# Kernel optimization log

Measured on AMD Instinct MI355X. Metric: run time of the kernel, lower is better.

The kernel has to match this reference:

```python
import math
import jax, jax.numpy as jnp
import numpy as np

B, DIM, L = 2, 512, 2048
H = 16
HD = DIM // H  # 32
R = 32
K = 3
GAMMA = 1.0


def _conv1d(x, w, b=None):
    # x: [B, Cin, L], w: [Cout, Cin, K] -> [B, Cout, L_out] (VALID)
    out = jax.lax.conv_general_dilated(
        x, w, window_strides=(1,), padding='VALID',
        dimension_numbers=('NCH', 'OIH', 'NCH'))
    if b is not None:
        out = out + b[None, :, None]
    return out


def _sketch_p4(x, G1, G2):
    # x: [B, H, L, HD]; G1, G2: [HD, R]
    # p=4: half = (1/sqrt(r)) * (x@G1 * x@G2); return half*half
    half = (x @ G1) * (x @ G2) / math.sqrt(R)
    return half * half  # [B, H, L, R]


def setup_inputs() -> dict:
    key = jax.random.key(0)
    ks = jax.random.split(key, 12)
    x = jax.random.normal(ks[0], (B, DIM, L), dtype=jnp.float32)
    # conv / linear params (kaiming-ish scale)
    q_w = jax.random.normal(ks[1], (DIM, DIM, K), dtype=jnp.float32) / math.sqrt(DIM * K)
    q_b = jnp.zeros((DIM,), dtype=jnp.float32)
    k_w = jax.random.normal(ks[2], (DIM, DIM, K), dtype=jnp.float32) / math.sqrt(DIM * K)
    k_b = jnp.zeros((DIM,), dtype=jnp.float32)
    v_w = jax.random.normal(ks[3], (DIM, DIM, 1), dtype=jnp.float32) / math.sqrt(DIM)
    proj_w = jax.random.normal(ks[4], (DIM, DIM), dtype=jnp.float32) / math.sqrt(DIM)
    proj_b = jnp.zeros((DIM,), dtype=jnp.float32)
    # learnable scalars
    gamma_q = jnp.ones((1,), dtype=jnp.float32) * GAMMA
    beta_q = jnp.zeros((1,), dtype=jnp.float32)
    gamma_k = jnp.ones((1,), dtype=jnp.float32) * GAMMA
    beta_k = jnp.zeros((1,), dtype=jnp.float32)
    # sketch matrices, std = 1/sqrt(r)
    G1q = jax.random.normal(ks[5], (HD, R), dtype=jnp.float32) / math.sqrt(R)
    G2q = jax.random.normal(ks[6], (HD, R), dtype=jnp.float32) / math.sqrt(R)
    G1k = jax.random.normal(ks[7], (HD, R), dtype=jnp.float32) / math.sqrt(R)
    G2k = jax.random.normal(ks[8], (HD, R), dtype=jnp.float32) / math.sqrt(R)
    return dict(x=x, q_w=q_w, q_b=q_b, k_w=k_w, k_b=k_b, v_w=v_w,
                proj_w=proj_w, proj_b=proj_b,
                gamma_q=gamma_q, beta_q=beta_q, gamma_k=gamma_k, beta_k=beta_k,
                G1q=G1q, G2q=G2q, G1k=G1k, G2k=G2k)


def reference(x, q_w, q_b, k_w, k_b, v_w, proj_w, proj_b,
              gamma_q, beta_q, gamma_k, beta_k, G1q, G2q, G1k, G2k):
    batch, dim, length = x.shape
    # causal left pad by K-1
    x_pad = jnp.pad(x, ((0, 0), (0, 0), (K - 1, 0)))
    q = _conv1d(x_pad, q_w, q_b)   # [B, DIM, L]
    k = _conv1d(x_pad, k_w, k_b)   # [B, DIM, L]
    v = _conv1d(x, v_w)            # [B, DIM, L] (1x1 conv, no bias)

    def shape(t):
        # [B, DIM, L] -> [B, H, HD, L] -> [B, H, L, HD]
        return t.reshape(batch, H, HD, length).transpose(0, 1, 3, 2)

    q, k, v = shape(q), shape(k), shape(v)
    q = gamma_q * q + beta_q
    k = gamma_k * k + beta_k
    phi_q = _sketch_p4(q, G1q, G2q)  # [B, H, L, R]
    phi_k = _sketch_p4(k, G1k, G2k)  # [B, H, L, R]
    scores = jnp.einsum('bhlr,bhmr->bhlm', phi_q, phi_k)  # [B, H, L, L]
    attn = scores / (scores.sum(axis=-1, keepdims=True) + 1e-6)
    o = jnp.einsum('bhlm,bhmd->bhld', attn, v)  # [B, H, L, HD]
    # [B, H, L, HD] -> [B, H, HD, L] -> [B, DIM, L] -> [B, L, DIM]
    o = o.transpose(0, 1, 3, 2).reshape(batch, dim, length).transpose(0, 2, 1)
    return o @ proj_w.T + proj_b
```

## Files before the change

### kernel.cpp

```cpp
#include <hip/hip_runtime.h>
#include <hip/hip_bf16.h>

#define DIMC 512
#define LEN  2048
#define NH   16
#define HD   32
#define RR   32

typedef __bf16 bf8_t __attribute__((ext_vector_type(8)));
typedef float  f4_t  __attribute__((ext_vector_type(4)));

__device__ __forceinline__ void gload16(const void* g, void* l) {
    __builtin_amdgcn_global_load_lds(
        (const __attribute__((address_space(1))) unsigned int*)g,
        (__attribute__((address_space(3))) unsigned int*)l, 16, 0, 0);
}

__global__ __launch_bounds__(256) void split_x_kernel(
    const float* __restrict__ x, __bf16* __restrict__ xTh, __bf16* __restrict__ xTl)
{
    __shared__ float tile[64][65];
    const int b  = blockIdx.z;
    const int l0 = blockIdx.x * 64;
    const int c0 = blockIdx.y * 64;
    const int tid = threadIdx.x;
    #pragma unroll
    for (int it = 0; it < 4; ++it) {
        int cl = (tid >> 4) + it * 16;
        int ll = (tid & 15) * 4;
        float4 v4 = *reinterpret_cast<const float4*>(
            x + ((size_t)b * DIMC + c0 + cl) * LEN + l0 + ll);
        tile[cl][ll+0] = v4.x; tile[cl][ll+1] = v4.y;
        tile[cl][ll+2] = v4.z; tile[cl][ll+3] = v4.w;
    }
    __syncthreads();
    const int lr = tid >> 2;
    const int cb = (tid & 3) * 16;
    size_t base = ((size_t)b * 2050 + l0 + lr + 2) * DIMC + c0 + cb;
    #pragma unroll
    for (int e = 0; e < 16; ++e) {
        float f = tile[cb + e][lr];
        __bf16 h = (__bf16)f;
        xTh[base + e] = h;
        xTl[base + e] = (__bf16)(f - (float)h);
    }
    if (blockIdx.x == 0 && blockIdx.y == 0) {
        size_t pb = (size_t)b * 2050 * DIMC;
        #pragma unroll
        for (int e = 0; e < 4; ++e) {
            int p = tid * 4 + e;
            xTh[pb + p] = (__bf16)0.f;
            xTl[pb + p] = (__bf16)0.f;
        }
    }
}

__global__ __launch_bounds__(256) void split_w_kernel(
    const float* __restrict__ qw, const float* __restrict__ kw,
    const float* __restrict__ vw, __bf16* __restrict__ Wrh, __bf16* __restrict__ Wrl)
{
    int idx = blockIdx.x * 256 + threadIdx.x;
    int m   = idx / 1536;
    int rem = idx - m * 1536;
    int kk  = rem >> 9;
    int ci  = rem & 511;
    float f;
    if (m < 512)       f = qw[((size_t)m * 512 + ci) * 3 + kk];
    else if (m < 1024) f = kw[((size_t)(m - 512) * 512 + ci) * 3 + kk];
    else               f = (kk == 2) ? vw[(size_t)(m - 1024) * 512 + ci] : 0.f;
    __bf16 h = (__bf16)f;
    Wrh[idx] = h;
    Wrl[idx] = (__bf16)(f - (float)h);
}

__global__ __launch_bounds__(256) void split_pw_kernel(
    const float* __restrict__ pw, __bf16* __restrict__ pwh, __bf16* __restrict__ pwl)
{
    int idx = blockIdx.x * 256 + threadIdx.x;
    float f = pw[idx];
    __bf16 h = (__bf16)f;
    pwh[idx] = h;
    pwl[idx] = (__bf16)(f - (float)h);
}

__global__ __launch_bounds__(256) void conv_mfma_kernel(
    const __bf16* __restrict__ xTh, const __bf16* __restrict__ xTl,
    const __bf16* __restrict__ Wrh, const __bf16* __restrict__ Wrl,
    const float* __restrict__ q_b, const float* __restrict__ k_b,
    float* __restrict__ q, float* __restrict__ k, float* __restrict__ v,
    int m_off, int kks)
{
    __shared__ __bf16 sAh[128 * 32], sAl[128 * 32], sBh[64 * 32], sBl[64 * 32];
    const int b   = blockIdx.z;
    const int mg  = m_off + blockIdx.y * 128;
    const int n0  = blockIdx.x * 64;
    const int tid = threadIdx.x;
    const int wave = tid >> 6, lane = tid & 63;
    const int wm = wave >> 1, wn = wave & 1;
    const int lr = lane & 15, k8 = lane >> 4;

    const __bf16* xh = xTh + (size_t)b * 2050 * DIMC;
    const __bf16* xl = xTl + (size_t)b * 2050 * DIMC;

    f4_t acc[4][2];
    #pragma unroll
    for (int i = 0; i < 4; ++i)
        #pragma unroll
        for (int j = 0; j < 2; ++j)
            #pragma unroll
            for (int e = 0; e < 4; ++e) acc[i][j][e] = 0.f;

    const int sr0 = tid >> 2;
    const int ss  = tid & 3;
    const int sk0 = ((ss ^ ((sr0 >> 1) & 3)) << 3);
    const int sr1 = sr0 + 64;
    const int sk1 = ((ss ^ ((sr1 >> 1) & 3)) << 3);

    for (int kk = kks; kk < 3; ++kk) {
        const __bf16* wAh = Wrh + (size_t)mg * 1536 + kk * 512;
        const __bf16* wAl = Wrl + (size_t)mg * 1536 + kk * 512;
        const __bf16* xbh = xh + (size_t)(n0 + kk) * DIMC;
        const __bf16* xbl = xl + (size_t)(n0 + kk) * DIMC;
        for (int k0 = 0; k0 < 512; k0 += 32) {
            gload16(wAh + (size_t)sr0 * 1536 + k0 + sk0, (char*)sAh + tid * 16);
            gload16(wAh + (size_t)sr1 * 1536 + k0 + sk1, (char*)sAh + (256 + tid) * 16);
            gload16(wAl + (size_t)sr0 * 1536 + k0 + sk0, (char*)sAl + tid * 16);
            gload16(wAl + (size_t)sr1 * 1536 + k0 + sk1, (char*)sAl + (256 + tid) * 16);
            gload16(xbh + (size_t)sr0 * DIMC + k0 + sk0, (char*)sBh + tid * 16);
            gload16(xbl + (size_t)sr0 * DIMC + k0 + sk0, (char*)sBl + tid * 16);
            __syncthreads();
            bf8_t ah[4], al[4], bh[2], bl[2];
            #pragma unroll
            for (int i = 0; i < 4; ++i) {
                int row = wm * 64 + i * 16 + lr;
                int off = row * 64 + ((k8 ^ ((row >> 1) & 3)) << 4);
                ah[i] = *(const bf8_t*)((const char*)sAh + off);
                al[i] = *(const bf8_t*)((const char*)sAl + off);
            }
            #pragma unroll
            for (int j = 0; j < 2; ++j) {
                int row = wn * 32 + j * 16 + lr;
                int off = row * 64 + ((k8 ^ ((row >> 1) & 3)) << 4);
                bh[j] = *(const bf8_t*)((const char*)sBh + off);
                bl[j] = *(const bf8_t*)((const char*)sBl + off);
            }
            #pragma unroll
            for (int i = 0; i < 4; ++i)
                #pragma unroll
                for (int j = 0; j < 2; ++j) {
                    acc[i][j] = __builtin_amdgcn_mfma_f32_16x16x32_bf16(ah[i], bh[j], acc[i][j], 0, 0, 0);
                    acc[i][j] = __builtin_amdgcn_mfma_f32_16x16x32_bf16(ah[i], bl[j], acc[i][j], 0, 0, 0);
                    acc[i][j] = __builtin_amdgcn_mfma_f32_16x16x32_bf16(al[i], bh[j], acc[i][j], 0, 0, 0);
                }
            __syncthreads();
        }
    }
    const int sec = mg >> 9;
    float* outp = (sec == 0) ? q : (sec == 1) ? k : v;
    const float* bp = (sec == 0) ? q_b : (sec == 1) ? k_b : nullptr;
    const int cob = mg & 511;
    #pragma unroll
    for (int i = 0; i < 4; ++i)
        #pragma unroll
        for (int r = 0; r < 4; ++r) {
            int co = cob + wm * 64 + i * 16 + k8 * 4 + r;
            float bv = bp ? bp[co] : 0.f;
            float* orow = outp + ((size_t)b * DIMC + co) * LEN;
            #pragma unroll
            for (int j = 0; j < 2; ++j)
                orow[n0 + wn * 32 + j * 16 + lr] = acc[i][j][r] + bv;
        }
}

__global__ __launch_bounds__(256) void proj_mfma_kernel(
    const __bf16* __restrict__ oh, const __bf16* __restrict__ ol,
    const __bf16* __restrict__ pwh, const __bf16* __restrict__ pwl,
    const float* __restrict__ pb, float* __restrict__ out)
{
    __shared__ __bf16 sAh[128 * 32], sAl[128 * 32], sBh[64 * 32], sBl[64 * 32];
    const int m0  = blockIdx.y * 128;
    const int n0  = blockIdx.x * 64;
    const int tid = threadIdx.x;
    const int wave = tid >> 6, lane = tid & 63;
    const int wm = wave >> 1, wn = wave & 1;
    const int lr = lane & 15, k8 = lane >> 4;

    f4_t acc[4][2];
    #pragma unroll
    for (int i = 0; i < 4; ++i)
        #pragma unroll
        for (int j = 0; j < 2; ++j)
            #pragma unroll
            for (int e = 0; e < 4; ++e) acc[i][j][e] = 0.f;

    const int sr0 = tid >> 2;
    const int ss  = tid & 3;
    const int sk0 = ((ss ^ ((sr0 >> 1) & 3)) << 3);
    const int sr1 = sr0 + 64;
    const int sk1 = ((ss ^ ((sr1 >> 1) & 3)) << 3);

    for (int k0 = 0; k0 < 512; k0 += 32) {
        gload16(oh + (size_t)(m0 + sr0) * DIMC + k0 + sk0, (char*)sAh + tid * 16);
        gload16(oh + (size_t)(m0 + sr1) * DIMC + k0 + sk1, (char*)sAh + (256 + tid) * 16);
        gload16(ol + (size_t)(m0 + sr0) * DIMC + k0 + sk0, (char*)sAl + tid * 16);
        gload16(ol + (size_t)(m0 + sr1) * DIMC + k0 + sk1, (char*)sAl + (256 + tid) * 16);
        gload16(pwh + (size_t)(n0 + sr0) * DIMC + k0 + sk0, (char*)sBh + tid * 16);
        gload16(pwl + (size_t)(n0 + sr0) * DIMC + k0 + sk0, (char*)sBl + tid * 16);
        __syncthreads();
        bf8_t ah[4], al[4], bh[2], bl[2];
        #pragma unroll
        for (int i = 0; i < 4; ++i) {
            int row = wm * 64 + i * 16 + lr;
            int off = row * 64 + ((k8 ^ ((row >> 1) & 3)) << 4);
            ah[i] = *(const bf8_t*)((const char*)sAh + off);
            al[i] = *(const bf8_t*)((const char*)sAl + off);
        }
        #pragma unroll
        for (int j = 0; j < 2; ++j) {
            int row = wn * 32 + j * 16 + lr;
            int off = row * 64 + ((k8 ^ ((row >> 1) & 3)) << 4);
            bh[j] = *(const bf8_t*)((const char*)sBh + off);
            bl[j] = *(const bf8_t*)((const char*)sBl + off);
        }
        #pragma unroll
        for (int i = 0; i < 4; ++i)
            #pragma unroll
            for (int j = 0; j < 2; ++j) {
                acc[i][j] = __builtin_amdgcn_mfma_f32_16x16x32_bf16(ah[i], bh[j], acc[i][j], 0, 0, 0);
                acc[i][j] = __builtin_amdgcn_mfma_f32_16x16x32_bf16(ah[i], bl[j], acc[i][j], 0, 0, 0);
                acc[i][j] = __builtin_amdgcn_mfma_f32_16x16x32_bf16(al[i], bh[j], acc[i][j], 0, 0, 0);
            }
        __syncthreads();
    }
    #pragma unroll
    for (int j = 0; j < 2; ++j) {
        int n = n0 + wn * 32 + j * 16 + lr;
        float bv = pb[n];
        #pragma unroll
        for (int i = 0; i < 4; ++i)
            #pragma unroll
            for (int r = 0; r < 4; ++r) {
                int m = m0 + wm * 64 + i * 16 + k8 * 4 + r;
                out[(size_t)m * DIMC + n] = acc[i][j][r] + bv;
            }
    }
}

__global__ __launch_bounds__(256) void sketch_kernel(
    const float* __restrict__ qk, const float* __restrict__ G1,
    const float* __restrict__ G2, const float* __restrict__ gamma,
    const float* __restrict__ beta, float* __restrict__ phi)
{
    __shared__ float g1s[HD][RR];
    __shared__ float g2s[HD][RR];
    __shared__ float qs[8][HD + 1];
    const int b = blockIdx.z, h = blockIdx.y;
    const int l0 = blockIdx.x * 8;
    const int tid = threadIdx.x;
    for (int i = tid; i < HD * RR; i += 256) {
        g1s[i >> 5][i & 31] = G1[i];
        g2s[i >> 5][i & 31] = G2[i];
    }
    const float ga = gamma[0], be = beta[0];
    {
        const int dd = tid >> 3, li = tid & 7;
        qs[li][dd] = ga * qk[((size_t)b * DIMC + h * HD + dd) * LEN + l0 + li] + be;
    }
    __syncthreads();
    const int r = tid & 31, li = tid >> 5;
    float a = 0.f, c = 0.f;
    #pragma unroll
    for (int dd = 0; dd < HD; ++dd) {
        float qv = qs[li][dd];
        a += qv * g1s[dd][r];
        c += qv * g2s[dd][r];
    }
    float hh = a * c * 0.17677669529663687f;
    phi[((size_t)(b * NH + h) * LEN + l0 + li) * RR + r] = hh * hh;
}

__global__ __launch_bounds__(256) void skv_kernel(
    const float* __restrict__ phi_k, const float* __restrict__ v,
    float* __restrict__ Skv, float* __restrict__ sk)
{
    const int b = blockIdx.z, h = blockIdx.y;
    const int l0 = blockIdx.x * 256;
    const int tid = threadIdx.x;
    __shared__ float ps[64][RR];
    __shared__ float vs[64][HD + 1];
    const int r  = tid >> 3;
    const int d4 = (tid & 7) * 4;
    float acc[4] = {0.f, 0.f, 0.f, 0.f};
    float skacc = 0.f;
    const float* pk = phi_k + ((size_t)(b * NH + h) * LEN + l0) * RR;
    const float* vb = v + ((size_t)b * DIMC + h * HD) * LEN + l0;
    for (int c = 0; c < 4; ++c) {
        for (int i = tid; i < 64 * 32; i += 256) {
            ps[i >> 5][i & 31] = pk[c * 64 * 32 + i];
            int dd = i >> 6, lc = i & 63;
            vs[lc][dd] = vb[(size_t)dd * LEN + c * 64 + lc];
        }
        __syncthreads();
        #pragma unroll 8
        for (int lc = 0; lc < 64; ++lc) {
            float pv = ps[lc][r];
            skacc += pv;
            #pragma unroll
            for (int j = 0; j < 4; ++j) acc[j] += pv * vs[lc][d4 + j];
        }
        __syncthreads();
    }
    const size_t base = (size_t)(b * NH + h) * RR + r;
    float* Sp = Skv + base * HD + d4;
    #pragma unroll
    for (int j = 0; j < 4; ++j) atomicAdd(Sp + j, acc[j]);
    if ((tid & 7) == 0) atomicAdd(sk + base, skacc);
}

__global__ __launch_bounds__(256) void onorm_kernel(
    const float* __restrict__ phi_q, const float* __restrict__ Skv,
    const float* __restrict__ sk, __bf16* __restrict__ o_h, __bf16* __restrict__ o_l)
{
    __shared__ float Ss[RR][HD];
    __shared__ float sks[RR];
    __shared__ float ph[8][RR + 1];
    const int b = blockIdx.z, hh = blockIdx.y;
    const int l0 = blockIdx.x * 8;
    const int tid = threadIdx.x;
    const int bh = b * NH + hh;
    for (int i = tid; i < RR * HD; i += 256) Ss[i >> 5][i & 31] = Skv[(size_t)bh * RR * HD + i];
    if (tid < RR) sks[tid] = sk[(size_t)bh * RR + tid];
    {
        const int r = tid & 31, li = tid >> 5;
        ph[li][r] = phi_q[((size_t)bh * LEN + l0 + li) * RR + r];
    }
    __syncthreads();
    const int d = tid & 31, li = tid >> 5;
    float num = 0.f, den = 0.f;
    #pragma unroll
    for (int r = 0; r < RR; ++r) {
        float p = ph[li][r];
        num += p * Ss[r][d];
        den += p * sks[r];
    }
    float val = num / (den + 1e-6f);
    __bf16 hv = (__bf16)val;
    size_t oi = ((size_t)b * LEN + l0 + li) * DIMC + hh * HD + d;
    o_h[oi] = hv;
    o_l[oi] = (__bf16)(val - (float)hv);
}

extern "C" void kernel_launch(void* const* d_in, const int* in_sizes, int n_in,
                              void* d_out, int out_size, void* d_ws, size_t ws_size,
                              hipStream_t stream)
{
    const float* x       = (const float*)d_in[0];
    const float* q_w     = (const float*)d_in[1];
    const float* q_b     = (const float*)d_in[2];
    const float* k_w     = (const float*)d_in[3];
    const float* k_b     = (const float*)d_in[4];
    const float* v_w     = (const float*)d_in[5];
    const float* proj_w  = (const float*)d_in[6];
    const float* proj_b  = (const float*)d_in[7];
    const float* gamma_q = (const float*)d_in[8];
    const float* beta_q  = (const float*)d_in[9];
    const float* gamma_k = (const float*)d_in[10];
    const float* beta_k  = (const float*)d_in[11];
    const float* G1q     = (const float*)d_in[12];
    const float* G2q     = (const float*)d_in[13];
    const float* G1k     = (const float*)d_in[14];
    const float* G2k     = (const float*)d_in[15];

    char* W = (char*)d_ws;
    constexpr size_t QKV   = (size_t)2 * DIMC * LEN * 4;
    constexpr size_t XT    = (size_t)2 * 2050 * DIMC * 2;
    constexpr size_t WR    = (size_t)1536 * 1536 * 2;
    constexpr size_t PW    = (size_t)DIMC * DIMC * 2;
    constexpr size_t SKVB  = (size_t)2 * NH * RR * HD * 4;
    constexpr size_t SKB   = (size_t)2 * NH * RR * 4;

    float*  q    = (float*)(W);
    float*  k    = (float*)(W + QKV);
    float*  v    = (float*)(W + 2 * QKV);
    __bf16* xTh  = (__bf16*)(W + 3 * QKV);
    __bf16* xTl  = (__bf16*)(W + 3 * QKV + XT);
    __bf16* Wrh  = (__bf16*)(W + 3 * QKV + 2 * XT);
    __bf16* Wrl  = (__bf16*)(W + 3 * QKV + 2 * XT + WR);
    __bf16* pwh  = (__bf16*)(W + 3 * QKV + 2 * XT + 2 * WR);
    __bf16* pwl  = (__bf16*)(W + 3 * QKV + 2 * XT + 2 * WR + PW);
    float*  Skv  = (float*)(W + 3 * QKV + 2 * XT + 2 * WR + 2 * PW);
    float*  sk   = (float*)(W + 3 * QKV + 2 * XT + 2 * WR + 2 * PW + SKVB);
    float*  phi_q = (float*)(W + 3 * QKV);
    float*  phi_k = (float*)(W + 3 * QKV + 2 * XT);
    __bf16* o_h   = (__bf16*)(W);
    __bf16* o_l   = (__bf16*)(W + QKV / 2);

    split_x_kernel<<<dim3(LEN / 64, DIMC / 64, 2), 256, 0, stream>>>(x, xTh, xTl);
    split_w_kernel<<<(1536 * 1536) / 256, 256, 0, stream>>>(q_w, k_w, v_w, Wrh, Wrl);
    split_pw_kernel<<<(DIMC * DIMC) / 256, 256, 0, stream>>>(proj_w, pwh, pwl);

    conv_mfma_kernel<<<dim3(LEN / 64, 8, 2), 256, 0, stream>>>(
        xTh, xTl, Wrh, Wrl, q_b, k_b, q, k, v, 0, 0);
    conv_mfma_kernel<<<dim3(LEN / 64, 4, 2), 256, 0, stream>>>(
        xTh, xTl, Wrh, Wrl, q_b, k_b, q, k, v, 1024, 2);

    dim3 sgrid(LEN / 8, NH, 2);
    sketch_kernel<<<sgrid, 256, 0, stream>>>(q, G1q, G2q, gamma_q, beta_q, phi_q);
    sketch_kernel<<<sgrid, 256, 0, stream>>>(k, G1k, G2k, gamma_k, beta_k, phi_k);

    hipMemsetAsync(Skv, 0, SKVB + SKB, stream);
    skv_kernel<<<dim3(LEN / 256, NH, 2), 256, 0, stream>>>(phi_k, v, Skv, sk);

    onorm_kernel<<<sgrid, 256, 0, stream>>>(phi_q, Skv, sk, o_h, o_l);

    proj_mfma_kernel<<<dim3(DIMC / 64, (2 * LEN) / 128), 256, 0, stream>>>(
        o_h, o_l, pwh, pwl, proj_b, (float*)d_out);
}
```

Baseline: 254.9 us.

## Fuse prep kernels and memset into one launch; fuse sketch into conv epilogue

```diff
diff --git a/kernel.cpp b/kernel.cpp
--- a/kernel.cpp
+++ b/kernel.cpp
@@ -16,88 +16,108 @@
         (__attribute__((address_space(3))) unsigned int*)l, 16, 0, 0);
 }
 
-__global__ __launch_bounds__(256) void split_x_kernel(
-    const float* __restrict__ x, __bf16* __restrict__ xTh, __bf16* __restrict__ xTl)
-{
-    __shared__ float tile[64][65];
-    const int b  = blockIdx.z;
-    const int l0 = blockIdx.x * 64;
-    const int c0 = blockIdx.y * 64;
+__global__ __launch_bounds__(256) void prep_kernel(
+    const float* __restrict__ x,
+    const float* __restrict__ qw, const float* __restrict__ kw,
+    const float* __restrict__ vw, const float* __restrict__ pw,
+    __bf16* __restrict__ xTh, __bf16* __restrict__ xTl,
+    __bf16* __restrict__ Wrh, __bf16* __restrict__ Wrl,
+    __bf16* __restrict__ pwh, __bf16* __restrict__ pwl,
+    float* __restrict__ Skv)
+{
+    const int bid = blockIdx.x;
     const int tid = threadIdx.x;
-    #pragma unroll
-    for (int it = 0; it < 4; ++it) {
-        int cl = (tid >> 4) + it * 16;
-        int ll = (tid & 15) * 4;
-        float4 v4 = *reinterpret_cast<const float4*>(
-            x + ((size_t)b * DIMC + c0 + cl) * LEN + l0 + ll);
-        tile[cl][ll+0] = v4.x; tile[cl][ll+1] = v4.y;
-        tile[cl][ll+2] = v4.z; tile[cl][ll+3] = v4.w;
-    }
-    __syncthreads();
-    const int lr = tid >> 2;
-    const int cb = (tid & 3) * 16;
-    size_t base = ((size_t)b * 2050 + l0 + lr + 2) * DIMC + c0 + cb;
-    #pragma unroll
-    for (int e = 0; e < 16; ++e) {
-        float f = tile[cb + e][lr];
+    if (bid < 512) {
+        __shared__ float tile[64][65];
+        const int lblk = bid & 31, cblk = (bid >> 5) & 7, b = bid >> 8;
+        const int l0 = lblk * 64, c0 = cblk * 64;
+        #pragma unroll
+        for (int it = 0; it < 4; ++it) {
+            int cl = (tid >> 4) + it * 16;
+            int ll = (tid & 15) * 4;
+            float4 v4 = *reinterpret_cast<const float4*>(
+                x + ((size_t)b * DIMC + c0 + cl) * LEN + l0 + ll);
+            tile[cl][ll+0] = v4.x; tile[cl][ll+1] = v4.y;
+            tile[cl][ll+2] = v4.z; tile[cl][ll+3] = v4.w;
+        }
+        __syncthreads();
+        const int l  = tid & 63;
+        const int cs = (tid >> 6) * 16;
+        size_t rowbase = ((size_t)b * 2050 + l0 + l + 2) * DIMC + c0;
+        #pragma unroll
+        for (int half = 0; half < 2; ++half) {
+            int c = cs + half * 8;
+            bf8_t hi, lo;
+            #pragma unroll
+            for (int e = 0; e < 8; ++e) {
+                float f = tile[c + e][l];
+                __bf16 h = (__bf16)f;
+                hi[e] = h;
+                lo[e] = (__bf16)(f - (float)h);
+            }
+            *reinterpret_cast<bf8_t*>(xTh + rowbase + c) = hi;
+            *reinterpret_cast<bf8_t*>(xTl + rowbase + c) = lo;
+        }
+        if (lblk == 0 && cblk == 0) {
+            size_t pb = (size_t)b * 2050 * DIMC;
+            #pragma unroll
+            for (int e = 0; e < 4; ++e) {
+                int p = tid * 4 + e;
+                xTh[pb + p] = (__bf16)0.f;
+                xTl[pb + p] = (__bf16)0.f;
+            }
+        }
+    } else if (bid < 9728) {
+        int idx = (bid - 512) * 256 + tid;
+        int m   = idx / 1536;
+        int rem = idx - m * 1536;
+        int kk  = rem >> 9;
+        int ci  = rem & 511;
+        float f;
+        if (m < 512)       f = qw[((size_t)m * 512 + ci) * 3 + kk];
+        else if (m < 1024) f = kw[((size_t)(m - 512) * 512 + ci) * 3 + kk];
+        else               f = (kk == 2) ? vw[(size_t)(m - 1024) * 512 + ci] : 0.f;
         __bf16 h = (__bf16)f;
-        xTh[base + e] = h;
-        xTl[base + e] = (__bf16)(f - (float)h);
-    }
-    if (blockIdx.x == 0 && blockIdx.y == 0) {
-        size_t pb = (size_t)b * 2050 * DIMC;
-        #pragma unroll
-        for (int e = 0; e < 4; ++e) {
-            int p = tid * 4 + e;
-            xTh[pb + p] = (__bf16)0.f;
-            xTl[pb + p] = (__bf16)0.f;
-        }
-    }
-}
-
-__global__ __launch_bounds__(256) void split_w_kernel(
-    const float* __restrict__ qw, const float* __restrict__ kw,
-    const float* __restrict__ vw, __bf16* __restrict__ Wrh, __bf16* __restrict__ Wrl)
-{
-    int idx = blockIdx.x * 256 + threadIdx.x;
-    int m   = idx / 1536;
-    int rem = idx - m * 1536;
-    int kk  = rem >> 9;
-    int ci  = rem & 511;
-    float f;
-    if (m < 512)       f = qw[((size_t)m * 512 + ci) * 3 + kk];
-    else if (m < 1024) f = kw[((size_t)(m - 512) * 512 + ci) * 3 + kk];
-    else               f = (kk == 2) ? vw[(size_t)(m - 1024) * 512 + ci] : 0.f;
-    __bf16 h = (__bf16)f;
-    Wrh[idx] = h;
-    Wrl[idx] = (__bf16)(f - (float)h);
-}
-
-__global__ __launch_bounds__(256) void split_pw_kernel(
-    const float* __restrict__ pw, __bf16* __restrict__ pwh, __bf16* __restrict__ pwl)
-{
-    int idx = blockIdx.x * 256 + threadIdx.x;
-    float f = pw[idx];
-    __bf16 h = (__bf16)f;
-    pwh[idx] = h;
-    pwl[idx] = (__bf16)(f - (float)h);
-}
-
-__global__ __launch_bounds__(256) void conv_mfma_kernel(
+        Wrh[idx] = h;
+        Wrl[idx] = (__bf16)(f - (float)h);
+    } else if (bid < 10752) {
+        int idx = (bid - 9728) * 256 + tid;
+        float f = pw[idx];
+        __bf16 h = (__bf16)f;
+        pwh[idx] = h;
+        pwl[idx] = (__bf16)(f - (float)h);
+    } else {
+        int idx = (bid - 10752) * 256 + tid;
+        if (idx < 33792) Skv[idx] = 0.f;
+    }
+}
+
+__global__ __launch_bounds__(256) void conv_sketch_kernel(
     const __bf16* __restrict__ xTh, const __bf16* __restrict__ xTl,
     const __bf16* __restrict__ Wrh, const __bf16* __restrict__ Wrl,
     const float* __restrict__ q_b, const float* __restrict__ k_b,
-    float* __restrict__ q, float* __restrict__ k, float* __restrict__ v,
-    int m_off, int kks)
-{
-    __shared__ __bf16 sAh[128 * 32], sAl[128 * 32], sBh[64 * 32], sBl[64 * 32];
+    const float* __restrict__ gamma_q, const float* __restrict__ beta_q,
+    const float* __restrict__ gamma_k, const float* __restrict__ beta_k,
+    const float* __restrict__ G1q, const float* __restrict__ G2q,
+    const float* __restrict__ G1k, const float* __restrict__ G2k,
+    float* __restrict__ phi_q, float* __restrict__ phi_k,
+    float* __restrict__ v)
+{
+    __shared__ __align__(16) char smem[24576];
+    __bf16* sAh = (__bf16*)(smem);
+    __bf16* sAl = (__bf16*)(smem + 8192);
+    __bf16* sBh = (__bf16*)(smem + 16384);
+    __bf16* sBl = (__bf16*)(smem + 20480);
+
     const int b   = blockIdx.z;
-    const int mg  = m_off + blockIdx.y * 128;
+    const int mg  = blockIdx.y * 128;
     const int n0  = blockIdx.x * 64;
     const int tid = threadIdx.x;
     const int wave = tid >> 6, lane = tid & 63;
     const int wm = wave >> 1, wn = wave & 1;
     const int lr = lane & 15, k8 = lane >> 4;
+    const int sec = mg >> 9;
+    const int kks = (sec == 2) ? 2 : 0;
 
     const __bf16* xh = xTh + (size_t)b * 2050 * DIMC;
     const __bf16* xl = xTl + (size_t)b * 2050 * DIMC;
@@ -155,128 +175,72 @@
             __syncthreads();
         }
     }
-    const int sec = mg >> 9;
-    float* outp = (sec == 0) ? q : (sec == 1) ? k : v;
-    const float* bp = (sec == 0) ? q_b : (sec == 1) ? k_b : nullptr;
+
     const int cob = mg & 511;
-    #pragma unroll
-    for (int i = 0; i < 4; ++i)
-        #pragma unroll
-        for (int r = 0; r < 4; ++r) {
-            int co = cob + wm * 64 + i * 16 + k8 * 4 + r;
-            float bv = bp ? bp[co] : 0.f;
-            float* orow = outp + ((size_t)b * DIMC + co) * LEN;
-            #pragma unroll
-            for (int j = 0; j < 2; ++j)
-                orow[n0 + wn * 32 + j * 16 + lr] = acc[i][j][r] + bv;
-        }
-}
-
-__global__ __launch_bounds__(256) void proj_mfma_kernel(
-    const __bf16* __restrict__ oh, const __bf16* __restrict__ ol,
-    const __bf16* __restrict__ pwh, const __bf16* __restrict__ pwl,
-    const float* __restrict__ pb, float* __restrict__ out)
-{
-    __shared__ __bf16 sAh[128 * 32], sAl[128 * 32], sBh[64 * 32], sBl[64 * 32];
-    const int m0  = blockIdx.y * 128;
-    const int n0  = blockIdx.x * 64;
-    const int tid = threadIdx.x;
-    const int wave = tid >> 6, lane = tid & 63;
-    const int wm = wave >> 1, wn = wave & 1;
-    const int lr = lane & 15, k8 = lane >> 4;
-
-    f4_t acc[4][2];
-    #pragma unroll
-    for (int i = 0; i < 4; ++i)
-        #pragma unroll
-        for (int j = 0; j < 2; ++j)
-            #pragma unroll
-            for (int e = 0; e < 4; ++e) acc[i][j][e] = 0.f;
-
-    const int sr0 = tid >> 2;
-    const int ss  = tid & 3;
-    const int sk0 = ((ss ^ ((sr0 >> 1) & 3)) << 3);
-    const int sr1 = sr0 + 64;
-    const int sk1 = ((ss ^ ((sr1 >> 1) & 3)) << 3);
-
-    for (int k0 = 0; k0 < 512; k0 += 32) {
-        gload16(oh + (size_t)(m0 + sr0) * DIMC + k0 + sk0, (char*)sAh + tid * 16);
-        gload16(oh + (size_t)(m0 + sr1) * DIMC + k0 + sk1, (char*)sAh + (256 + tid) * 16);
-        gload16(ol + (size_t)(m0 + sr0) * DIMC + k0 + sk0, (char*)sAl + tid * 16);
-        gload16(ol + (size_t)(m0 + sr1) * DIMC + k0 + sk1, (char*)sAl + (256 + tid) * 16);
-        gload16(pwh + (size_t)(n0 + sr0) * DIMC + k0 + sk0, (char*)sBh + tid * 16);
-        gload16(pwl + (size_t)(n0 + sr0) * DIMC + k0 + sk0, (char*)sBl + tid * 16);
-        __syncthreads();
-        bf8_t ah[4], al[4], bh[2], bl[2];
-        #pragma unroll
-        for (int i = 0; i < 4; ++i) {
-            int row = wm * 64 + i * 16 + lr;
-            int off = row * 64 + ((k8 ^ ((row >> 1) & 3)) << 4);
-            ah[i] = *(const bf8_t*)((const char*)sAh + off);
-            al[i] = *(const bf8_t*)((const char*)sAl + off);
-        }
-        #pragma unroll
-        for (int j = 0; j < 2; ++j) {
-            int row = wn * 32 + j * 16 + lr;
-            int off = row * 64 + ((k8 ^ ((row >> 1) & 3)) << 4);
-            bh[j] = *(const bf8_t*)((const char*)sBh + off);
-            bl[j] = *(const bf8_t*)((const char*)sBl + off);
-        }
+    if (sec == 2) {
         #pragma unroll
         for (int i = 0; i < 4; ++i)
             #pragma unroll
-            for (int j = 0; j < 2; ++j) {
-                acc[i][j] = __builtin_amdgcn_mfma_f32_16x16x32_bf16(ah[i], bh[j], acc[i][j], 0, 0, 0);
-                acc[i][j] = __builtin_amdgcn_mfma_f32_16x16x32_bf16(ah[i], bl[j], acc[i][j], 0, 0, 0);
-                acc[i][j] = __builtin_amdgcn_mfma_f32_16x16x32_bf16(al[i], bh[j], acc[i][j], 0, 0, 0);
-            }
-        __syncthreads();
-    }
-    #pragma unroll
-    for (int j = 0; j < 2; ++j) {
-        int n = n0 + wn * 32 + j * 16 + lr;
-        float bv = pb[n];
-        #pragma unroll
-        for (int i = 0; i < 4; ++i)
-            #pragma unroll
             for (int r = 0; r < 4; ++r) {
-                int m = m0 + wm * 64 + i * 16 + k8 * 4 + r;
-                out[(size_t)m * DIMC + n] = acc[i][j][r] + bv;
-            }
-    }
-}
-
-__global__ __launch_bounds__(256) void sketch_kernel(
-    const float* __restrict__ qk, const float* __restrict__ G1,
-    const float* __restrict__ G2, const float* __restrict__ gamma,
-    const float* __restrict__ beta, float* __restrict__ phi)
-{
-    __shared__ float g1s[HD][RR];
-    __shared__ float g2s[HD][RR];
-    __shared__ float qs[8][HD + 1];
-    const int b = blockIdx.z, h = blockIdx.y;
-    const int l0 = blockIdx.x * 8;
-    const int tid = threadIdx.x;
-    for (int i = tid; i < HD * RR; i += 256) {
-        g1s[i >> 5][i & 31] = G1[i];
-        g2s[i >> 5][i & 31] = G2[i];
-    }
-    const float ga = gamma[0], be = beta[0];
-    {
-        const int dd = tid >> 3, li = tid & 7;
-        qs[li][dd] = ga * qk[((size_t)b * DIMC + h * HD + dd) * LEN + l0 + li] + be;
-    }
-    __syncthreads();
-    const int r = tid & 31, li = tid >> 5;
-    float a = 0.f, c = 0.f;
-    #pragma unroll
-    for (int dd = 0; dd < HD; ++dd) {
-        float qv = qs[li][dd];
-        a += qv * g1s[dd][r];
-        c += qv * g2s[dd][r];
-    }
-    float hh = a * c * 0.17677669529663687f;
-    phi[((size_t)(b * NH + h) * LEN + l0 + li) * RR + r] = hh * hh;
+                int co = cob + wm * 64 + i * 16 + k8 * 4 + r;
+                float* orow = v + ((size_t)b * DIMC + co) * LEN;
+                #pragma unroll
+                for (int j = 0; j < 2; ++j)
+                    orow[n0 + wn * 32 + j * 16 + lr] = acc[i][j][r];
+            }
+        return;
+    }
+
+    const float* G1 = (sec == 0) ? G1q : G1k;
+    const float* G2 = (sec == 0) ? G2q : G2k;
+    const float* bp = (sec == 0) ? q_b : k_b;
+    const float ga  = (sec == 0) ? gamma_q[0] : gamma_k[0];
+    const float be  = (sec == 0) ? beta_q[0]  : beta_k[0];
+    float* phi      = (sec == 0) ? phi_q : phi_k;
+
+    const int r = lane & 31;
+    float g1r[32], g2r[32];
+    #pragma unroll
+    for (int d = 0; d < 32; ++d) {
+        g1r[d] = G1[d * 32 + r];
+        g2r[d] = G2[d * 32 + r];
+    }
+    float* q_s = (float*)smem;
+    const int hb = cob >> 5;
+    const int hl = wave >> 1;
+    const int lbase = (wave & 1) * 32 + (lane >> 5) * 16;
+
+    #pragma unroll
+    for (int p = 0; p < 2; ++p) {
+        if (wm == p) {
+            #pragma unroll
+            for (int i = 0; i < 4; ++i)
+                #pragma unroll
+                for (int rr = 0; rr < 4; ++rr) {
+                    int lrow = i * 16 + k8 * 4 + rr;
+                    float bv = bp[cob + p * 64 + lrow];
+                    #pragma unroll
+                    for (int j = 0; j < 2; ++j)
+                        q_s[lrow * 66 + wn * 32 + j * 16 + lr] =
+                            ga * (acc[i][j][rr] + bv) + be;
+                }
+        }
+        __syncthreads();
+        const int h = hb + 2 * p + hl;
+        for (int t = 0; t < 16; ++t) {
+            int lloc = lbase + t;
+            float a = 0.f, cc = 0.f;
+            #pragma unroll
+            for (int d = 0; d < 32; ++d) {
+                float qv = q_s[(hl * 32 + d) * 66 + lloc];
+                a  += qv * g1r[d];
+                cc += qv * g2r[d];
+            }
+            float hh = a * cc * 0.17677669529663687f;
+            phi[(((size_t)b * NH + h) * LEN + n0 + lloc) * RR + r] = hh * hh;
+        }
+        __syncthreads();
+    }
 }
 
 __global__ __launch_bounds__(256) void skv_kernel(
@@ -350,6 +314,80 @@
     o_l[oi] = (__bf16)(val - (float)hv);
 }
 
+__global__ __launch_bounds__(256) void proj_mfma_kernel(
+    const __bf16* __restrict__ oh, const __bf16* __restrict__ ol,
+    const __bf16* __restrict__ pwh, const __bf16* __restrict__ pwl,
+    const float* __restrict__ pb, float* __restrict__ out)
+{
+    __shared__ __bf16 sAh[128 * 32], sAl[128 * 32], sBh[64 * 32], sBl[64 * 32];
+    const int m0  = blockIdx.y * 128;
+    const int n0  = blockIdx.x * 64;
+    const int tid = threadIdx.x;
+    const int wave = tid >> 6, lane = tid & 63;
+    const int wm = wave >> 1, wn = wave & 1;
+    const int lr = lane & 15, k8 = lane >> 4;
+
+    f4_t acc[4][2];
+    #pragma unroll
+    for (int i = 0; i < 4; ++i)
+        #pragma unroll
+        for (int j = 0; j < 2; ++j)
+            #pragma unroll
+            for (int e = 0; e < 4; ++e) acc[i][j][e] = 0.f;
+
+    const int sr0 = tid >> 2;
+    const int ss  = tid & 3;
+    const int sk0 = ((ss ^ ((sr0 >> 1) & 3)) << 3);
+    const int sr1 = sr0 + 64;
+    const int sk1 = ((ss ^ ((sr1 >> 1) & 3)) << 3);
+
+    for (int k0 = 0; k0 < 512; k0 += 32) {
+        gload16(oh + (size_t)(m0 + sr0) * DIMC + k0 + sk0, (char*)sAh + tid * 16);
+        gload16(oh + (size_t)(m0 + sr1) * DIMC + k0 + sk1, (char*)sAh + (256 + tid) * 16);
+        gload16(ol + (size_t)(m0 + sr0) * DIMC + k0 + sk0, (char*)sAl + tid * 16);
+        gload16(ol + (size_t)(m0 + sr1) * DIMC + k0 + sk1, (char*)sAl + (256 + tid) * 16);
+        gload16(pwh + (size_t)(n0 + sr0) * DIMC + k0 + sk0, (char*)sBh + tid * 16);
+        gload16(pwl + (size_t)(n0 + sr0) * DIMC + k0 + sk0, (char*)sBl + tid * 16);
+        __syncthreads();
+        bf8_t ah[4], al[4], bh[2], bl[2];
+        #pragma unroll
+        for (int i = 0; i < 4; ++i) {
+            int row = wm * 64 + i * 16 + lr;
+            int off = row * 64 + ((k8 ^ ((row >> 1) & 3)) << 4);
+            ah[i] = *(const bf8_t*)((const char*)sAh + off);
+            al[i] = *(const bf8_t*)((const char*)sAl + off);
+        }
+        #pragma unroll
+        for (int j = 0; j < 2; ++j) {
+            int row = wn * 32 + j * 16 + lr;
+            int off = row * 64 + ((k8 ^ ((row >> 1) & 3)) << 4);
+            bh[j] = *(const bf8_t*)((const char*)sBh + off);
+            bl[j] = *(const bf8_t*)((const char*)sBl + off);
+        }
+        #pragma unroll
+        for (int i = 0; i < 4; ++i)
+            #pragma unroll
+            for (int j = 0; j < 2; ++j) {
+                acc[i][j] = __builtin_amdgcn_mfma_f32_16x16x32_bf16(ah[i], bh[j], acc[i][j], 0, 0, 0);
+                acc[i][j] = __builtin_amdgcn_mfma_f32_16x16x32_bf16(ah[i], bl[j], acc[i][j], 0, 0, 0);
+                acc[i][j] = __builtin_amdgcn_mfma_f32_16x16x32_bf16(al[i], bh[j], acc[i][j], 0, 0, 0);
+            }
+        __syncthreads();
+    }
+    #pragma unroll
+    for (int j = 0; j < 2; ++j) {
+        int n = n0 + wn * 32 + j * 16 + lr;
+        float bv = pb[n];
+        #pragma unroll
+        for (int i = 0; i < 4; ++i)
+            #pragma unroll
+            for (int r = 0; r < 4; ++r) {
+                int m = m0 + wm * 64 + i * 16 + k8 * 4 + r;
+                out[(size_t)m * DIMC + n] = acc[i][j][r] + bv;
+            }
+    }
+}
+
 extern "C" void kernel_launch(void* const* d_in, const int* in_sizes, int n_in,
                               void* d_out, int out_size, void* d_ws, size_t ws_size,
                               hipStream_t stream)
@@ -372,46 +410,36 @@
     const float* G2k     = (const float*)d_in[15];
 
     char* W = (char*)d_ws;
-    constexpr size_t QKV   = (size_t)2 * DIMC * LEN * 4;
-    constexpr size_t XT    = (size_t)2 * 2050 * DIMC * 2;
-    constexpr size_t WR    = (size_t)1536 * 1536 * 2;
-    constexpr size_t PW    = (size_t)DIMC * DIMC * 2;
-    constexpr size_t SKVB  = (size_t)2 * NH * RR * HD * 4;
-    constexpr size_t SKB   = (size_t)2 * NH * RR * 4;
-
-    float*  q    = (float*)(W);
-    float*  k    = (float*)(W + QKV);
-    float*  v    = (float*)(W + 2 * QKV);
-    __bf16* xTh  = (__bf16*)(W + 3 * QKV);
-    __bf16* xTl  = (__bf16*)(W + 3 * QKV + XT);
-    __bf16* Wrh  = (__bf16*)(W + 3 * QKV + 2 * XT);
-    __bf16* Wrl  = (__bf16*)(W + 3 * QKV + 2 * XT + WR);
-    __bf16* pwh  = (__bf16*)(W + 3 * QKV + 2 * XT + 2 * WR);
-    __bf16* pwl  = (__bf16*)(W + 3 * QKV + 2 * XT + 2 * WR + PW);
-    float*  Skv  = (float*)(W + 3 * QKV + 2 * XT + 2 * WR + 2 * PW);
-    float*  sk   = (float*)(W + 3 * QKV + 2 * XT + 2 * WR + 2 * PW + SKVB);
-    float*  phi_q = (float*)(W + 3 * QKV);
-    float*  phi_k = (float*)(W + 3 * QKV + 2 * XT);
-    __bf16* o_h   = (__bf16*)(W);
-    __bf16* o_l   = (__bf16*)(W + QKV / 2);
-
-    split_x_kernel<<<dim3(LEN / 64, DIMC / 64, 2), 256, 0, stream>>>(x, xTh, xTl);
-    split_w_kernel<<<(1536 * 1536) / 256, 256, 0, stream>>>(q_w, k_w, v_w, Wrh, Wrl);
-    split_pw_kernel<<<(DIMC * DIMC) / 256, 256, 0, stream>>>(proj_w, pwh, pwl);
-
-    conv_mfma_kernel<<<dim3(LEN / 64, 8, 2), 256, 0, stream>>>(
-        xTh, xTl, Wrh, Wrl, q_b, k_b, q, k, v, 0, 0);
-    conv_mfma_kernel<<<dim3(LEN / 64, 4, 2), 256, 0, stream>>>(
-        xTh, xTl, Wrh, Wrl, q_b, k_b, q, k, v, 1024, 2);
-
-    dim3 sgrid(LEN / 8, NH, 2);
-    sketch_kernel<<<sgrid, 256, 0, stream>>>(q, G1q, G2q, gamma_q, beta_q, phi_q);
-    sketch_kernel<<<sgrid, 256, 0, stream>>>(k, G1k, G2k, gamma_k, beta_k, phi_k);
-
-    hipMemsetAsync(Skv, 0, SKVB + SKB, stream);
+    constexpr size_t VB   = (size_t)2 * DIMC * LEN * 4;
+    constexpr size_t XT   = (size_t)2 * 2050 * DIMC * 2;
+    constexpr size_t WR   = (size_t)1536 * 1536 * 2;
+    constexpr size_t PW   = (size_t)DIMC * DIMC * 2;
+    constexpr size_t PHI  = (size_t)2 * NH * LEN * RR * 4;
+
+    float*  v    = (float*)(W);
+    __bf16* xTh  = (__bf16*)(W + VB);
+    __bf16* xTl  = (__bf16*)(W + VB + XT);
+    __bf16* Wrh  = (__bf16*)(W + VB + 2 * XT);
+    __bf16* Wrl  = (__bf16*)(W + VB + 2 * XT + WR);
+    __bf16* pwh  = (__bf16*)(W + VB + 2 * XT + 2 * WR);
+    __bf16* pwl  = (__bf16*)(W + VB + 2 * XT + 2 * WR + PW);
+    float*  phi_q = (float*)(W + VB + 2 * XT + 2 * WR + 2 * PW);
+    float*  phi_k = (float*)(W + VB + 2 * XT + 2 * WR + 2 * PW + PHI);
+    float*  Skv  = (float*)(W + VB + 2 * XT + 2 * WR + 2 * PW + 2 * PHI);
+    float*  sk   = Skv + (size_t)2 * NH * RR * HD;
+    __bf16* o_h  = xTh;
+    __bf16* o_l  = (__bf16*)(W + VB + XT);
+
+    prep_kernel<<<10884, 256, 0, stream>>>(x, q_w, k_w, v_w, proj_w,
+                                           xTh, xTl, Wrh, Wrl, pwh, pwl, Skv);
+
+    conv_sketch_kernel<<<dim3(LEN / 64, 12, 2), 256, 0, stream>>>(
+        xTh, xTl, Wrh, Wrl, q_b, k_b, gamma_q, beta_q, gamma_k, beta_k,
+        G1q, G2q, G1k, G2k, phi_q, phi_k, v);
+
     skv_kernel<<<dim3(LEN / 256, NH, 2), 256, 0, stream>>>(phi_k, v, Skv, sk);
 
-    onorm_kernel<<<sgrid, 256, 0, stream>>>(phi_q, Skv, sk, o_h, o_l);
+    onorm_kernel<<<dim3(LEN / 8, NH, 2), 256, 0, stream>>>(phi_q, Skv, sk, o_h, o_l);
 
     proj_mfma_kernel<<<dim3(DIMC / 64, (2 * LEN) / 128), 256, 0, stream>>>(
         o_h, o_l, pwh, pwl, proj_b, (float*)d_out);
```

New measurement: 261.4 us. 1.03x slower.
